# Optimization experiments

Hardware: AMD Instinct MI355X
Metric: run time of the kernel (lower is better)

Reference implementation:

```python
import jax, jax.numpy as jnp
import numpy as np

B, T, D = 2, 2048, 1024
H, DH = 16, 64  # heads, head_dim; inner_dim = H*DH = D
EPS = 1e-6


def _rmsnorm(x, g):
    # torch.nn.RMSNorm over last dim with affine weight g
    return x * jax.lax.rsqrt(jnp.mean(x * x, axis=-1, keepdims=True) + EPS) * g


def _interleaved_rope(x, cos, sin):
    # x: [B, T, D]; pairs (x0, x1) rotated: rot = [-x1, x0, -x3, x2, ...]
    b, t, d = x.shape
    x2 = x.reshape(b, t, d // 2, 2)
    rot = jnp.stack([-x2[..., 1], x2[..., 0]], axis=-1).reshape(b, t, d)
    return x * cos + rot * sin


def setup_inputs() -> dict:
    key = jax.random.key(0)
    ks = jax.random.split(key, 8)
    hidden_states = jax.random.normal(ks[0], (B, T, D), dtype=jnp.float32)
    cos = jax.random.uniform(ks[1], (1, T, D), dtype=jnp.float32)
    sin = jax.random.uniform(ks[2], (1, T, D), dtype=jnp.float32)
    s = 0.02  # init scale for weights
    wq = jax.random.normal(ks[3], (D, D), dtype=jnp.float32) * s
    wk = jax.random.normal(ks[4], (D, D), dtype=jnp.float32) * s
    wv = jax.random.normal(ks[5], (D, D), dtype=jnp.float32) * s
    wo = jax.random.normal(ks[6], (D, D), dtype=jnp.float32) * s
    bq = jnp.zeros((D,), jnp.float32)
    bk = jnp.zeros((D,), jnp.float32)
    bv = jnp.zeros((D,), jnp.float32)
    bo = jnp.zeros((D,), jnp.float32)
    gq = jnp.ones((D,), jnp.float32)
    gk = jnp.ones((D,), jnp.float32)
    return {
        'hidden_states': hidden_states, 'cos': cos, 'sin': sin,
        'wq': wq, 'bq': bq, 'wk': wk, 'bk': bk, 'wv': wv, 'bv': bv,
        'gq': gq, 'gk': gk, 'wo': wo, 'bo': bo,
    }


def reference(hidden_states, cos, sin, wq, bq, wk, bk, wv, bv, gq, gk, wo, bo):
    # QKV projections (weights stored as [in, out]) + RMSNorm(q,k) + RoPE
    q = _interleaved_rope(_rmsnorm(hidden_states @ wq + bq, gq), cos, sin)
    k = _interleaved_rope(_rmsnorm(hidden_states @ wk + bk, gk), cos, sin)
    v = hidden_states @ wv + bv

    # split heads: [B, T, D] -> [B, H, T, DH]
    def split(x):
        return x.reshape(B, T, H, DH).transpose(0, 2, 1, 3)
    q, k, v = split(q), split(k), split(v)

    scale = 1.0 / jnp.sqrt(jnp.float32(DH))
    scores = jnp.einsum('bhqd,bhkd->bhqk', q, k) * scale
    attn = jax.nn.softmax(scores, axis=-1)
    out = jnp.einsum('bhqk,bhkd->bhqd', attn, v)

    # merge heads + output projection
    out = out.transpose(0, 2, 1, 3).reshape(B, T, D)
    return out @ wo + bo
```

## Files before the change

### kernel.cpp

```cpp
#include <hip/hip_runtime.h>

typedef _Float16 f16;
typedef _Float16 f16x8 __attribute__((ext_vector_type(8)));
typedef _Float16 f16x4 __attribute__((ext_vector_type(4)));
typedef _Float16 f16x2 __attribute__((ext_vector_type(2)));
typedef float f32x4 __attribute__((ext_vector_type(4)));

#define MFMA(a, b, c) __builtin_amdgcn_mfma_f32_16x16x32_f16(a, b, c, 0, 0, 0)
#define PKRTZ(a, b) __builtin_bit_cast(f16x2, __builtin_amdgcn_cvt_pkrtz(a, b))

__device__ __forceinline__ void gload16(const void* g, void* l) {
  __builtin_amdgcn_global_load_lds((const __attribute__((address_space(1))) char*)g,
                                   (__attribute__((address_space(3))) char*)l, 16, 0, 0);
}


__global__ __launch_bounds__(256) void k_cvt_hidden(const float* __restrict__ x, f16* __restrict__ y) {
  int i = blockIdx.x * 256 + threadIdx.x;
  float4 v = ((const float4*)x)[i];
  f16x4 h; h[0] = (f16)v.x; h[1] = (f16)v.y; h[2] = (f16)v.z; h[3] = (f16)v.w;
  ((f16x4*)y)[i] = h;
}

__global__ __launch_bounds__(256) void k_cvt_w(const float* __restrict__ w0, const float* __restrict__ w1,
                                               const float* __restrict__ w2, const float* __restrict__ w3,
                                               f16* __restrict__ wt) {
  int z = blockIdx.z;
  const float* w = z == 0 ? w0 : z == 1 ? w1 : z == 2 ? w2 : w3;
  f16* dst = wt + (size_t)z * 1024 * 1024;
  __shared__ float tile[64][65];
  int t = threadIdx.x;
  int k0 = blockIdx.x * 64, n0 = blockIdx.y * 64;
  int cr = t >> 4, cc = (t & 15) * 4;
#pragma unroll
  for (int p = 0; p < 4; p++) {
    int r = cr + p * 16;
    float4 v = *(const float4*)&w[(size_t)(k0 + r) * 1024 + n0 + cc];
    tile[r][cc + 0] = v.x; tile[r][cc + 1] = v.y; tile[r][cc + 2] = v.z; tile[r][cc + 3] = v.w;
  }
  __syncthreads();
#pragma unroll
  for (int p = 0; p < 4; p++) {
    int nn = cr + p * 16;
    f16x4 h;
    h[0] = (f16)tile[cc + 0][nn]; h[1] = (f16)tile[cc + 1][nn];
    h[2] = (f16)tile[cc + 2][nn]; h[3] = (f16)tile[cc + 3][nn];
    *(f16x4*)&dst[(size_t)(n0 + nn) * 1024 + k0 + cc] = h;
  }
}

template <bool OUTF32>
__device__ __forceinline__ void gemm_core(const f16* __restrict__ A, const f16* __restrict__ Wrows,
                                          const float* __restrict__ bias, int m0,
                                          f16* __restrict__ oh, float* __restrict__ of) {
  __shared__ f16 Al[2][128 * 64];
  __shared__ f16 Bl[2][128 * 64];
  const int t = threadIdx.x;
  const int lane = t & 63, wid = t >> 6;
  const int lr = lane & 15, lg = lane >> 4;
  const int wm = wid >> 1, wn = wid & 1;
  const int lrow = lane >> 3;
  const int cb = (((lane & 7) ^ lrow) << 4);

  f32x4 acc[4][4] = {};

  auto stage = [&](int k0, int bs) {
#pragma unroll
    for (int it = 0; it < 4; it++) {
      int rbase = it * 32 + wid * 8;
      int row = rbase + lrow;
      gload16((const char*)&A[(size_t)(m0 + row) * 1024 + k0] + cb, (char*)&Al[bs][0] + rbase * 128);
      gload16((const char*)&Wrows[(size_t)row * 1024 + k0] + cb, (char*)&Bl[bs][0] + rbase * 128);
    }
  };

  stage(0, 0);
  __syncthreads();
  int cur = 0;
  for (int k0 = 0; k0 < 1024; k0 += 64) {
    if (k0 + 64 < 1024) stage(k0 + 64, cur ^ 1);
    f16x8 af[2][4], bf[2][4];
#pragma unroll
    for (int x = 0; x < 4; x++) {
      int ra = wm * 64 + x * 16 + lr;
      int rb = wn * 64 + x * 16 + lr;
#pragma unroll
      for (int kh = 0; kh < 2; kh++) {
        int ca = (kh * 64 + lg * 16) ^ ((lr & 7) << 4);
        af[kh][x] = *(const f16x8*)((char*)&Al[cur][0] + ra * 128 + ca);
        bf[kh][x] = *(const f16x8*)((char*)&Bl[cur][0] + rb * 128 + ca);
      }
    }
    __builtin_amdgcn_s_setprio(1);
#pragma unroll
    for (int kh = 0; kh < 2; kh++)
#pragma unroll
      for (int mt = 0; mt < 4; mt++)
#pragma unroll
        for (int nt = 0; nt < 4; nt++)
          acc[mt][nt] = MFMA(af[kh][mt], bf[kh][nt], acc[mt][nt]);
    __builtin_amdgcn_s_setprio(0);
    __syncthreads();
    cur ^= 1;
  }
#pragma unroll
  for (int mt = 0; mt < 4; mt++) {
#pragma unroll
    for (int nt = 0; nt < 4; nt++) {
      int col = wn * 64 + nt * 16 + lr;
      float bcol = bias[col];
#pragma unroll
      for (int e = 0; e < 4; e++) {
        int row = m0 + wm * 64 + mt * 16 + lg * 4 + e;
        float val = acc[mt][nt][e] + bcol;
        if (OUTF32) of[(size_t)row * 1024 + col] = val;
        else        oh[(size_t)row * 1024 + col] = (f16)val;
      }
    }
  }
}

__global__ __launch_bounds__(256, 2) void k_gemm_qkv(const f16* __restrict__ A, const f16* __restrict__ wt,
                                                     const float* __restrict__ bq, const float* __restrict__ bk,
                                                     const float* __restrict__ bv,
                                                     f16* __restrict__ q, f16* __restrict__ k, f16* __restrict__ v) {
  int n0 = blockIdx.y * 128;
  int zsel = n0 >> 10, cbs = n0 & 1023;
  const float* bias = (zsel == 0 ? bq : zsel == 1 ? bk : bv) + cbs;
  f16* dst = (zsel == 0 ? q : zsel == 1 ? k : v) + cbs;
  gemm_core<false>(A, wt + (size_t)n0 * 1024, bias, blockIdx.x * 128, dst, nullptr);
}

__global__ __launch_bounds__(256, 2) void k_gemm_o(const f16* __restrict__ A, const f16* __restrict__ wt3,
                                                   const float* __restrict__ bo, float* __restrict__ out) {
  int n0 = blockIdx.y * 128;
  gemm_core<true>(A, wt3 + (size_t)n0 * 1024, bo + n0, blockIdx.x * 128, nullptr, out + n0);
}

__global__ __launch_bounds__(256) void k_normrope(f16* __restrict__ qh, f16* __restrict__ kh,
                                                  const float* __restrict__ gq, const float* __restrict__ gk,
                                                  const float* __restrict__ cs, const float* __restrict__ sn) {
  int row = blockIdx.x, which = blockIdx.y;
  f16* buf = which ? kh : qh;
  const float* g = which ? gk : gq;
  int t = threadIdx.x, c4 = t * 4;
  f16x4 xv = *(const f16x4*)&buf[(size_t)row * 1024 + c4];
  float x0 = xv[0], x1 = xv[1], x2 = xv[2], x3 = xv[3];
  float ss = x0 * x0 + x1 * x1 + x2 * x2 + x3 * x3;
#pragma unroll
  for (int off = 1; off < 64; off <<= 1) ss += __shfl_xor(ss, off);
  __shared__ float red[4];
  if ((t & 63) == 0) red[t >> 6] = ss;
  __syncthreads();
  float inv = rsqrtf((red[0] + red[1] + red[2] + red[3]) * (1.0f / 1024.0f) + 1e-6f);
  int tt = row & 2047;
  float4 cv = *(const float4*)&cs[(size_t)tt * 1024 + c4];
  float4 sv = *(const float4*)&sn[(size_t)tt * 1024 + c4];
  float4 gv = *(const float4*)&g[c4];
  float y0 = x0 * inv * gv.x, y1 = x1 * inv * gv.y, y2 = x2 * inv * gv.z, y3 = x3 * inv * gv.w;
  f16x4 ov;
  ov[0] = (f16)(y0 * cv.x - y1 * sv.x);
  ov[1] = (f16)(y1 * cv.y + y0 * sv.y);
  ov[2] = (f16)(y2 * cv.z - y3 * sv.z);
  ov[3] = (f16)(y3 * cv.w + y2 * sv.w);
  *(f16x4*)&buf[(size_t)row * 1024 + c4] = ov;
}

__global__ __launch_bounds__(256) void k_vtrans(const f16* __restrict__ vh, f16* __restrict__ vt) {
  __shared__ f16 tile[64][65];
  int t = threadIdx.x;
  int t0 = blockIdx.x * 64;
  int bh = blockIdx.y;
  int b = bh >> 4, h = bh & 15;
  int rr = t >> 3, c8 = (t & 7) * 8;
#pragma unroll
  for (int p = 0; p < 2; p++) {
    int r = p * 32 + rr;
    f16x8 v = *(const f16x8*)&vh[(size_t)(b * 2048 + t0 + r) * 1024 + h * 64 + c8];
#pragma unroll
    for (int j = 0; j < 8; j++) tile[r][c8 + j] = v[j];
  }
  __syncthreads();
#pragma unroll
  for (int p = 0; p < 2; p++) {
    int dh = p * 32 + rr;
    f16x8 o;
#pragma unroll
    for (int j = 0; j < 8; j++) o[j] = tile[c8 + j][dh];
    *(f16x8*)&vt[((size_t)bh * 64 + dh) * 2048 + t0 + c8] = o;
  }
}

#define ASWZ(row) ((((row) & 3) | (((row) & 8) >> 1)) << 4)

__global__ __launch_bounds__(256, 2) void k_attn(const f16* __restrict__ qh, const f16* __restrict__ kh,
                                                 const f16* __restrict__ vt, f16* __restrict__ ao) {
  __shared__ f16 Kl[2][64 * 64];
  __shared__ f16 Vl[2][64 * 64];
  const int t = threadIdx.x;
  const int lane = t & 63, wid = t >> 6;
  const int lr = lane & 15, lg = lane >> 4;
  const int lgb = lg << 4;
  const int raw = blockIdx.x;
  const int mybh = ((raw & 7) << 2) | ((raw >> 3) & 3);
  const int myq = raw >> 5;
  const int b = mybh >> 4, h = mybh & 15;
  const int q0 = myq * 128 + wid * 32;
  const f16* Qb = qh + ((size_t)(b * 2048 + q0)) * 1024 + h * 64;
  f16x8 qf[2][2];
#pragma unroll
  for (int g = 0; g < 2; g++) {
    qf[g][0] = *(const f16x8*)&Qb[(size_t)(g * 16 + lr) * 1024 + lg * 8];
    qf[g][1] = *(const f16x8*)&Qb[(size_t)(g * 16 + lr) * 1024 + 32 + lg * 8];
  }
  const f16* Kg = kh + ((size_t)b * 2048) * 1024 + h * 64;
  const f16* Vg = vt + ((size_t)mybh) * 64 * 2048;
  const int lrow = lane >> 3;
  const int sg = (lane & 7) << 4;
  const float sc = 0.125f * 1.44269504088896340736f;
  float m[2] = {-1e30f, -1e30f};
  f32x4 acc[2][4] = {};
  f32x4 accl[2] = {};
  const f16 ov1 = (lr == 0) ? (f16)1.0f : (f16)0.0f;
  const f16x8 onesf = {ov1, ov1, ov1, ov1, ov1, ov1, ov1, ov1};

  auto stage = [&](int kvo, int bs) {
#pragma unroll
    for (int i = 0; i < 2; i++) {
      int rbase = (i * 4 + wid) * 8;
      int row = rbase + lrow;
      int cswz = sg ^ ASWZ(row);
      gload16((const char*)(Kg + (size_t)(kvo + row) * 1024) + cswz, (char*)&Kl[bs][0] + rbase * 128);
      gload16((const char*)(Vg + (size_t)row * 2048 + kvo) + cswz, (char*)&Vl[bs][0] + rbase * 128);
    }
  };

  stage(0, 0);
  __syncthreads();
  int cur = 0;

  for (int kv0 = 0; kv0 < 2048; kv0 += 64) {
    if (kv0 + 64 < 2048) stage(kv0 + 64, cur ^ 1);
    const char* Kb = (const char*)&Kl[cur][0];
    const char* Vb = (const char*)&Vl[cur][0];

    f32x4 s[2][4];
    __builtin_amdgcn_s_setprio(1);
#pragma unroll
    for (int ks = 0; ks < 4; ks++) {
      int key = ((lr >> 2) << 3) + (lr & 3) + ((ks & 1) << 2) + ((ks >> 1) << 5);
      int sw = ASWZ(key);
      f16x8 kf0 = *(const f16x8*)(Kb + key * 128 + (lgb ^ sw));
      f16x8 kf1 = *(const f16x8*)(Kb + key * 128 + ((64 + lgb) ^ sw));
#pragma unroll
      for (int g = 0; g < 2; g++) {
        f32x4 z = {};
        z = MFMA(kf0, qf[g][0], z);
        z = MFMA(kf1, qf[g][1], z);
        s[g][ks] = z;
      }
    }
    __builtin_amdgcn_s_setprio(0);

    union U { f16x8 v; f16x2 h[4]; } u[2][2];
#pragma unroll
    for (int g = 0; g < 2; g++) {
      float smax = fmaxf(fmaxf(s[g][0][0], s[g][0][1]), s[g][0][2]);
      smax = fmaxf(fmaxf(smax, s[g][0][3]), s[g][1][0]);
      smax = fmaxf(fmaxf(smax, s[g][1][1]), s[g][1][2]);
      smax = fmaxf(fmaxf(smax, s[g][1][3]), s[g][2][0]);
      smax = fmaxf(fmaxf(smax, s[g][2][1]), s[g][2][2]);
      smax = fmaxf(fmaxf(smax, s[g][2][3]), s[g][3][0]);
      smax = fmaxf(fmaxf(smax, s[g][3][1]), s[g][3][2]);
      smax = fmaxf(smax, s[g][3][3]);
      smax = fmaxf(smax, __shfl_xor(smax, 16));
      smax = fmaxf(smax, __shfl_xor(smax, 32));
      float smc = smax * sc;

      if (!__all(smc - m[g] <= 8.f)) {
        float mn = fmaxf(m[g], smc);
        float al = exp2f(m[g] - mn);
        m[g] = mn;
        float alq[4];
#pragma unroll
        for (int e = 0; e < 4; e++) alq[e] = __shfl(al, lg * 4 + e);
#pragma unroll
        for (int ds = 0; ds < 4; ds++)
#pragma unroll
          for (int e = 0; e < 4; e++) acc[g][ds][e] *= alq[e];
#pragma unroll
        for (int e = 0; e < 4; e++) accl[g][e] *= alq[e];
      }

#pragma unroll
      for (int ks = 0; ks < 4; ks++) {
        float p0 = exp2f(fmaf(s[g][ks][0], sc, -m[g]));
        float p1 = exp2f(fmaf(s[g][ks][1], sc, -m[g]));
        float p2 = exp2f(fmaf(s[g][ks][2], sc, -m[g]));
        float p3 = exp2f(fmaf(s[g][ks][3], sc, -m[g]));
        u[g][ks >> 1].h[(ks & 1) * 2 + 0] = PKRTZ(p0, p1);
        u[g][ks >> 1].h[(ks & 1) * 2 + 1] = PKRTZ(p2, p3);
      }
    }

    __builtin_amdgcn_s_setprio(1);
#pragma unroll
    for (int ds = 0; ds < 4; ds++) {
      int vrow = ds * 16 + lr;
      int sw = ASWZ(vrow);
      f16x8 vf0 = *(const f16x8*)(Vb + vrow * 128 + (lgb ^ sw));
      f16x8 vf1 = *(const f16x8*)(Vb + vrow * 128 + ((64 + lgb) ^ sw));
#pragma unroll
      for (int g = 0; g < 2; g++) {
        acc[g][ds] = MFMA(u[g][0].v, vf0, acc[g][ds]);
        acc[g][ds] = MFMA(u[g][1].v, vf1, acc[g][ds]);
      }
    }
#pragma unroll
    for (int g = 0; g < 2; g++) {
      accl[g] = MFMA(u[g][0].v, onesf, accl[g]);
      accl[g] = MFMA(u[g][1].v, onesf, accl[g]);
    }
    __builtin_amdgcn_s_setprio(0);

    __syncthreads();
    cur ^= 1;
  }

#pragma unroll
  for (int g = 0; g < 2; g++) {
#pragma unroll
    for (int e = 0; e < 4; e++) {
      float lf = 1.f / __shfl(accl[g][e], lg << 4);
      size_t row = (size_t)(b * 2048 + q0 + g * 16 + lg * 4 + e);
#pragma unroll
      for (int ds = 0; ds < 4; ds++)
        ao[row * 1024 + h * 64 + ds * 16 + lr] = (f16)(acc[g][ds][e] * lf);
    }
  }
}

extern "C" void kernel_launch(void* const* d_in, const int* in_sizes, int n_in,
                              void* d_out, int out_size, void* d_ws, size_t ws_size,
                              hipStream_t stream) {
  const float* hid  = (const float*)d_in[0];
  const float* cosb = (const float*)d_in[1];
  const float* sinb = (const float*)d_in[2];
  const float* wq = (const float*)d_in[3];
  const float* bq = (const float*)d_in[4];
  const float* wk = (const float*)d_in[5];
  const float* bk = (const float*)d_in[6];
  const float* wv = (const float*)d_in[7];
  const float* bv = (const float*)d_in[8];
  const float* gq = (const float*)d_in[9];
  const float* gk = (const float*)d_in[10];
  const float* wo = (const float*)d_in[11];
  const float* bo = (const float*)d_in[12];
  float* out = (float*)d_out;

  char* ws = (char*)d_ws;
  f16* aH  = (f16*)(ws);
  f16* wt  = (f16*)(ws + ((size_t)8 << 20));
  f16* qh  = (f16*)(ws + ((size_t)16 << 20));
  f16* khb = (f16*)(ws + ((size_t)24 << 20));
  f16* vhb = (f16*)(ws + ((size_t)32 << 20));
  f16* vtb = (f16*)(ws + ((size_t)40 << 20));
  f16* ao  = (f16*)(ws + ((size_t)48 << 20));

  k_cvt_hidden<<<dim3(4096), dim3(256), 0, stream>>>(hid, aH);
  k_cvt_w<<<dim3(16, 16, 4), dim3(256), 0, stream>>>(wq, wk, wv, wo, wt);
  k_gemm_qkv<<<dim3(32, 24), dim3(256), 0, stream>>>(aH, wt, bq, bk, bv, qh, khb, vhb);
  k_normrope<<<dim3(4096, 2), dim3(256), 0, stream>>>(qh, khb, gq, gk, cosb, sinb);
  k_vtrans<<<dim3(32, 32), dim3(256), 0, stream>>>(vhb, vtb);
  k_attn<<<dim3(512), dim3(256), 0, stream>>>(qh, khb, vtb, ao);
  k_gemm_o<<<dim3(32, 8), dim3(256), 0, stream>>>(ao, wt + (size_t)3 * 1024 * 1024, bo, out);
}
```

Measured before the change: 143.2 us.

## Split attention KV range in two halves and merge partials with log-sum-exp

The attention kernel now splits each query tile's key/value range into two halves handled by separate blocks, doubling the grid from 512 to 1024 blocks and raising the occupancy hint to 4 blocks per SM. Each half writes a normalized partial output plus its running max and row sum, and a new merge kernel combines the two halves with log-sum-exp weights. The aim is to fill more of the GPU's compute units during attention. The cost is an extra kernel launch, extra global traffic for the partial outputs (stored in reused workspace buffers), and possible register spilling under the tighter launch bounds.

Measured after the change: 145.1 us. No clear change (+1.3%).

```diff
diff --git a/kernel.cpp b/kernel.cpp
--- a/kernel.cpp
+++ b/kernel.cpp
@@ -193,8 +193,10 @@
 
 #define ASWZ(row) ((((row) & 3) | (((row) & 8) >> 1)) << 4)
 
-__global__ __launch_bounds__(256, 2) void k_attn(const f16* __restrict__ qh, const f16* __restrict__ kh,
-                                                 const f16* __restrict__ vt, f16* __restrict__ ao) {
+__global__ __launch_bounds__(256, 4) void k_attn(const f16* __restrict__ qh, const f16* __restrict__ kh,
+                                                 const f16* __restrict__ vt,
+                                                 f16* __restrict__ op0, f16* __restrict__ op1,
+                                                 float* __restrict__ ml) {
   __shared__ f16 Kl[2][64 * 64];
   __shared__ f16 Vl[2][64 * 64];
   const int t = threadIdx.x;
@@ -203,9 +205,12 @@
   const int lgb = lg << 4;
   const int raw = blockIdx.x;
   const int mybh = ((raw & 7) << 2) | ((raw >> 3) & 3);
-  const int myq = raw >> 5;
+  const int half = (raw >> 5) & 1;
+  const int myq = raw >> 6;
   const int b = mybh >> 4, h = mybh & 15;
   const int q0 = myq * 128 + wid * 32;
+  const int kvbase = half << 10;
+  f16* __restrict__ op = half ? op1 : op0;
   const f16* Qb = qh + ((size_t)(b * 2048 + q0)) * 1024 + h * 64;
   f16x8 qf[2][2];
 #pragma unroll
@@ -235,12 +240,13 @@
     }
   };
 
-  stage(0, 0);
+  stage(kvbase, 0);
   __syncthreads();
   int cur = 0;
 
-  for (int kv0 = 0; kv0 < 2048; kv0 += 64) {
-    if (kv0 + 64 < 2048) stage(kv0 + 64, cur ^ 1);
+  for (int c = 0; c < 16; c++) {
+    int kv0 = kvbase + c * 64;
+    if (c + 1 < 16) stage(kv0 + 64, cur ^ 1);
     const char* Kb = (const char*)&Kl[cur][0];
     const char* Vb = (const char*)&Vl[cur][0];
 
@@ -329,15 +335,43 @@
 
 #pragma unroll
   for (int g = 0; g < 2; g++) {
+    int qglob = mybh * 2048 + q0 + g * 16;
+    if (lg == 0)
+      ml[(size_t)((half << 16) + qglob + lr) * 2 + 0] = m[g];
+    if (lr == 0) {
+#pragma unroll
+      for (int e = 0; e < 4; e++)
+        ml[(size_t)((half << 16) + qglob + lg * 4 + e) * 2 + 1] = accl[g][e];
+    }
 #pragma unroll
     for (int e = 0; e < 4; e++) {
       float lf = 1.f / __shfl(accl[g][e], lg << 4);
       size_t row = (size_t)(b * 2048 + q0 + g * 16 + lg * 4 + e);
 #pragma unroll
       for (int ds = 0; ds < 4; ds++)
-        ao[row * 1024 + h * 64 + ds * 16 + lr] = (f16)(acc[g][ds][e] * lf);
-    }
-  }
+        op[row * 1024 + h * 64 + ds * 16 + lr] = (f16)(acc[g][ds][e] * lf);
+    }
+  }
+}
+
+__global__ __launch_bounds__(256) void k_merge(const f16* __restrict__ op0, const f16* __restrict__ op1,
+                                               const float* __restrict__ ml, f16* __restrict__ ao) {
+  int i = blockIdx.x * 256 + threadIdx.x;
+  int qid = i >> 3, seg = i & 7;
+  float m0 = ml[(size_t)qid * 2], l0 = ml[(size_t)qid * 2 + 1];
+  float m1 = ml[(size_t)(65536 + qid) * 2], l1 = ml[(size_t)(65536 + qid) * 2 + 1];
+  float mm = fmaxf(m0, m1);
+  float w0 = l0 * exp2f(m0 - mm), w1 = l1 * exp2f(m1 - mm);
+  float inv = 1.f / (w0 + w1);
+  w0 *= inv; w1 *= inv;
+  int bh = qid >> 11, tt = qid & 2047;
+  size_t addr = (((size_t)(bh >> 4) * 2048 + tt) * 1024 + (bh & 15) * 64 + seg * 8) / 8;
+  f16x8 a = ((const f16x8*)op0)[addr];
+  f16x8 bb = ((const f16x8*)op1)[addr];
+  f16x8 o;
+#pragma unroll
+  for (int j = 0; j < 8; j++) o[j] = (f16)(w0 * (float)a[j] + w1 * (float)bb[j]);
+  ((f16x8*)ao)[addr] = o;
 }
 
 extern "C" void kernel_launch(void* const* d_in, const int* in_sizes, int n_in,
@@ -366,12 +400,14 @@
   f16* vhb = (f16*)(ws + ((size_t)32 << 20));
   f16* vtb = (f16*)(ws + ((size_t)40 << 20));
   f16* ao  = (f16*)(ws + ((size_t)48 << 20));
+  float* ml = (float*)(ws + ((size_t)56 << 20));
 
   k_cvt_hidden<<<dim3(4096), dim3(256), 0, stream>>>(hid, aH);
   k_cvt_w<<<dim3(16, 16, 4), dim3(256), 0, stream>>>(wq, wk, wv, wo, wt);
   k_gemm_qkv<<<dim3(32, 24), dim3(256), 0, stream>>>(aH, wt, bq, bk, bv, qh, khb, vhb);
   k_normrope<<<dim3(4096, 2), dim3(256), 0, stream>>>(qh, khb, gq, gk, cosb, sinb);
   k_vtrans<<<dim3(32, 32), dim3(256), 0, stream>>>(vhb, vtb);
-  k_attn<<<dim3(512), dim3(256), 0, stream>>>(qh, khb, vtb, ao);
+  k_attn<<<dim3(1024), dim3(256), 0, stream>>>(qh, khb, vtb, vhb, aH, ml);
+  k_merge<<<dim3(2048), dim3(256), 0, stream>>>(vhb, aH, ml, ao);
   k_gemm_o<<<dim3(32, 8), dim3(256), 0, stream>>>(ao, wt + (size_t)3 * 1024 * 1024, bo, out);
 }
```

## Rewrite QKV GEMM as 256x256 tile with 8-wave ping-pong LDS pipeline

Applied to the files above, without the earlier changes.

The QKV projection GEMM moves from 128x128 tiles with 4 waves and double buffering to 256x256 tiles with 8 waves. Each tile is split into four 128-row half-tiles per K step, and global-to-LDS loads are interleaved with MFMA quadrants under explicit barriers and waitcnts. A block-index swizzle groups neighbouring tiles for L2 reuse. The aim is to raise data reuse per LDS byte and hide load latency. The costs are a grid of only 192 blocks on 256 CUs (under one wave of work) and a fragile hand-written synchronisation schedule.

Result: no change. 142.8 us (-0.3%).

```diff
diff --git a/kernel.cpp b/kernel.cpp
--- a/kernel.cpp
+++ b/kernel.cpp
@@ -8,6 +8,8 @@
 
 #define MFMA(a, b, c) __builtin_amdgcn_mfma_f32_16x16x32_f16(a, b, c, 0, 0, 0)
 #define PKRTZ(a, b) __builtin_bit_cast(f16x2, __builtin_amdgcn_cvt_pkrtz(a, b))
+#define BARRAW() do { asm volatile("" ::: "memory"); __builtin_amdgcn_s_barrier(); asm volatile("" ::: "memory"); } while (0)
+#define WAITLGKM0() do { asm volatile("s_waitcnt lgkmcnt(0)" ::: "memory"); __builtin_amdgcn_sched_barrier(0); } while (0)
 
 __device__ __forceinline__ void gload16(const void* g, void* l) {
   __builtin_amdgcn_global_load_lds((const __attribute__((address_space(1))) char*)g,
@@ -49,10 +51,144 @@
   }
 }
 
-template <bool OUTF32>
-__device__ __forceinline__ void gemm_core(const f16* __restrict__ A, const f16* __restrict__ Wrows,
-                                          const float* __restrict__ bias, int m0,
-                                          f16* __restrict__ oh, float* __restrict__ of) {
+__global__ __launch_bounds__(512, 1) void k_gemm_qkv(const f16* __restrict__ A, const f16* __restrict__ wt,
+                                                     const float* __restrict__ bq, const float* __restrict__ bk,
+                                                     const float* __restrict__ bv,
+                                                     f16* __restrict__ q, f16* __restrict__ k, f16* __restrict__ v) {
+  __shared__ f16 L[8][128 * 64];
+  const int t = threadIdx.x;
+  const int lane = t & 63, wid = t >> 6;
+  const int lr = lane & 15, lg = lane >> 4;
+  const int wm = wid >> 2, wn = wid & 3;
+  const int lrow = lane >> 3;
+  const int cb = (((lane & 7) ^ lrow) << 4);
+  const int bid = blockIdx.x;
+  const int x = bid & 7, loc = bid >> 3;
+  const int bx = (x & 3) * 4 + (loc & 3);
+  const int by = (x >> 2) * 6 + (loc >> 2);
+  const int m0 = bx * 256, n0 = by * 256;
+  const f16* Ag = A + (size_t)m0 * 1024;
+  const f16* Wr = wt + (size_t)n0 * 1024;
+  const int zsel = by >> 2, cbs = (by & 3) * 256;
+  const float* bias = (zsel == 0 ? bq : zsel == 1 ? bk : bv) + cbs;
+  f16* dst = (zsel == 0 ? q : zsel == 1 ? k : v) + cbs;
+
+  f32x4 acc[8][4] = {};
+
+  auto stageH = [&](int par, int mat, int h, int tk) {
+    const f16* base = (mat ? Wr : Ag) + (size_t)(h * 128) * 1024 + (tk << 6);
+    char* slot = (char*)&L[par * 4 + mat * 2 + h][0];
+#pragma unroll
+    for (int j = 0; j < 2; j++) {
+      int rbase = j * 64 + wid * 8;
+      gload16((const char*)&base[(size_t)(rbase + lrow) * 1024] + cb, slot + rbase * 128);
+    }
+  };
+  auto loadA = [&](int par, int h, f16x8 (&af)[8]) {
+    const char* S = (const char*)&L[par * 4 + h][0];
+#pragma unroll
+    for (int mt = 0; mt < 4; mt++) {
+      int ra = wm * 64 + mt * 16 + lr;
+#pragma unroll
+      for (int kh = 0; kh < 2; kh++)
+        af[mt * 2 + kh] = *(const f16x8*)(S + ra * 128 + ((kh * 64 + lg * 16) ^ ((lr & 7) << 4)));
+    }
+  };
+  auto loadB = [&](int par, int h, f16x8 (&bf)[4]) {
+    const char* S = (const char*)&L[par * 4 + 2 + h][0];
+#pragma unroll
+    for (int nt = 0; nt < 2; nt++) {
+      int rb = wn * 32 + nt * 16 + lr;
+#pragma unroll
+      for (int kh = 0; kh < 2; kh++)
+        bf[nt * 2 + kh] = *(const f16x8*)(S + rb * 128 + ((kh * 64 + lg * 16) ^ ((lr & 7) << 4)));
+    }
+  };
+  auto mfma16 = [&](int mh, int nh, f16x8 (&af)[8], f16x8 (&bf)[4]) {
+    __builtin_amdgcn_s_setprio(1);
+#pragma unroll
+    for (int kh = 0; kh < 2; kh++)
+#pragma unroll
+      for (int mt = 0; mt < 4; mt++)
+#pragma unroll
+        for (int nt = 0; nt < 2; nt++)
+          acc[mh * 4 + mt][nh * 2 + nt] = MFMA(af[mt * 2 + kh], bf[nt * 2 + kh], acc[mh * 4 + mt][nh * 2 + nt]);
+    __builtin_amdgcn_s_setprio(0);
+  };
+
+  stageH(0, 0, 0, 0); stageH(0, 1, 0, 0); stageH(0, 1, 1, 0); stageH(0, 0, 1, 0);
+  stageH(1, 0, 0, 1); stageH(1, 1, 1, 1); stageH(1, 0, 1, 1);
+  asm volatile("s_waitcnt vmcnt(6)" ::: "memory");
+  BARRAW();
+
+  f16x8 afA[8], afB[8], bfA[4], bfB[4];
+  for (int i = 0; i < 8; i++) {
+    const int t2 = 2 * i + 2, t3 = 2 * i + 3;
+    const bool pre = (i < 7);
+    loadA(0, 0, afA); loadB(0, 0, bfA);
+    stageH(1, 1, 0, 2 * i + 1);
+    BARRAW(); WAITLGKM0();
+    mfma16(0, 0, afA, bfA);
+    BARRAW();
+    loadB(0, 1, bfB);
+    if (pre) stageH(0, 0, 0, t2);
+    BARRAW(); WAITLGKM0();
+    mfma16(0, 1, afA, bfB);
+    BARRAW();
+    loadA(0, 1, afB);
+    if (pre) stageH(0, 1, 1, t2);
+    BARRAW(); WAITLGKM0();
+    mfma16(1, 1, afB, bfB);
+    BARRAW();
+    loadB(0, 0, bfA);
+    if (pre) stageH(0, 0, 1, t2);
+    asm volatile("s_waitcnt vmcnt(4)" ::: "memory");
+    BARRAW(); WAITLGKM0();
+    mfma16(1, 0, afB, bfA);
+    BARRAW();
+    loadA(1, 0, afA); loadB(1, 0, bfA);
+    if (pre) stageH(0, 1, 0, t2);
+    BARRAW(); WAITLGKM0();
+    mfma16(0, 0, afA, bfA);
+    BARRAW();
+    loadB(1, 1, bfB);
+    if (pre) stageH(1, 0, 0, t3);
+    BARRAW(); WAITLGKM0();
+    mfma16(0, 1, afA, bfB);
+    BARRAW();
+    loadA(1, 1, afB);
+    if (pre) stageH(1, 1, 1, t3);
+    BARRAW(); WAITLGKM0();
+    mfma16(1, 1, afB, bfB);
+    BARRAW();
+    loadB(1, 0, bfA);
+    if (pre) stageH(1, 0, 1, t3);
+    asm volatile("s_waitcnt vmcnt(4)" ::: "memory");
+    BARRAW(); WAITLGKM0();
+    mfma16(1, 0, afB, bfA);
+    BARRAW();
+  }
+
+#pragma unroll
+  for (int mh = 0; mh < 2; mh++)
+#pragma unroll
+    for (int mt = 0; mt < 4; mt++)
+#pragma unroll
+      for (int nh = 0; nh < 2; nh++)
+#pragma unroll
+        for (int nt = 0; nt < 2; nt++) {
+          int col = nh * 128 + wn * 32 + nt * 16 + lr;
+          float bcol = bias[col];
+#pragma unroll
+          for (int e = 0; e < 4; e++) {
+            int row = m0 + mh * 128 + wm * 64 + mt * 16 + lg * 4 + e;
+            dst[(size_t)row * 1024 + col] = (f16)(acc[mh * 4 + mt][nh * 2 + nt][e] + bcol);
+          }
+        }
+}
+
+__global__ __launch_bounds__(256, 2) void k_gemm_o(const f16* __restrict__ A, const f16* __restrict__ Wrows3,
+                                                   const float* __restrict__ bo, float* __restrict__ out) {
   __shared__ f16 Al[2][128 * 64];
   __shared__ f16 Bl[2][128 * 64];
   const int t = threadIdx.x;
@@ -61,6 +197,10 @@
   const int wm = wid >> 1, wn = wid & 1;
   const int lrow = lane >> 3;
   const int cb = (((lane & 7) ^ lrow) << 4);
+  const int m0 = blockIdx.x * 128, n0 = blockIdx.y * 128;
+  const f16* Wrows = Wrows3 + (size_t)n0 * 1024;
+  const float* bias = bo + n0;
+  float* of = out + n0;
 
   f32x4 acc[4][4] = {};
 
@@ -81,14 +221,14 @@
     if (k0 + 64 < 1024) stage(k0 + 64, cur ^ 1);
     f16x8 af[2][4], bf[2][4];
 #pragma unroll
-    for (int x = 0; x < 4; x++) {
-      int ra = wm * 64 + x * 16 + lr;
-      int rb = wn * 64 + x * 16 + lr;
+    for (int xx = 0; xx < 4; xx++) {
+      int ra = wm * 64 + xx * 16 + lr;
+      int rb = wn * 64 + xx * 16 + lr;
 #pragma unroll
       for (int kh = 0; kh < 2; kh++) {
         int ca = (kh * 64 + lg * 16) ^ ((lr & 7) << 4);
-        af[kh][x] = *(const f16x8*)((char*)&Al[cur][0] + ra * 128 + ca);
-        bf[kh][x] = *(const f16x8*)((char*)&Bl[cur][0] + rb * 128 + ca);
+        af[kh][xx] = *(const f16x8*)((char*)&Al[cur][0] + ra * 128 + ca);
+        bf[kh][xx] = *(const f16x8*)((char*)&Bl[cur][0] + rb * 128 + ca);
       }
     }
     __builtin_amdgcn_s_setprio(1);
@@ -112,29 +252,10 @@
 #pragma unroll
       for (int e = 0; e < 4; e++) {
         int row = m0 + wm * 64 + mt * 16 + lg * 4 + e;
-        float val = acc[mt][nt][e] + bcol;
-        if (OUTF32) of[(size_t)row * 1024 + col] = val;
-        else        oh[(size_t)row * 1024 + col] = (f16)val;
-      }
-    }
-  }
-}
-
-__global__ __launch_bounds__(256, 2) void k_gemm_qkv(const f16* __restrict__ A, const f16* __restrict__ wt,
-                                                     const float* __restrict__ bq, const float* __restrict__ bk,
-                                                     const float* __restrict__ bv,
-                                                     f16* __restrict__ q, f16* __restrict__ k, f16* __restrict__ v) {
-  int n0 = blockIdx.y * 128;
-  int zsel = n0 >> 10, cbs = n0 & 1023;
-  const float* bias = (zsel == 0 ? bq : zsel == 1 ? bk : bv) + cbs;
-  f16* dst = (zsel == 0 ? q : zsel == 1 ? k : v) + cbs;
-  gemm_core<false>(A, wt + (size_t)n0 * 1024, bias, blockIdx.x * 128, dst, nullptr);
-}
-
-__global__ __launch_bounds__(256, 2) void k_gemm_o(const f16* __restrict__ A, const f16* __restrict__ wt3,
-                                                   const float* __restrict__ bo, float* __restrict__ out) {
-  int n0 = blockIdx.y * 128;
-  gemm_core<true>(A, wt3 + (size_t)n0 * 1024, bo + n0, blockIdx.x * 128, nullptr, out + n0);
+        of[(size_t)row * 1024 + col] = acc[mt][nt][e] + bcol;
+      }
+    }
+  }
 }
 
 __global__ __launch_bounds__(256) void k_normrope(f16* __restrict__ qh, f16* __restrict__ kh,
@@ -369,7 +490,7 @@
 
   k_cvt_hidden<<<dim3(4096), dim3(256), 0, stream>>>(hid, aH);
   k_cvt_w<<<dim3(16, 16, 4), dim3(256), 0, stream>>>(wq, wk, wv, wo, wt);
-  k_gemm_qkv<<<dim3(32, 24), dim3(256), 0, stream>>>(aH, wt, bq, bk, bv, qh, khb, vhb);
+  k_gemm_qkv<<<dim3(192), dim3(512), 0, stream>>>(aH, wt, bq, bk, bv, qh, khb, vhb);
   k_normrope<<<dim3(4096, 2), dim3(256), 0, stream>>>(qh, khb, gq, gk, cosb, sinb);
   k_vtrans<<<dim3(32, 32), dim3(256), 0, stream>>>(vhb, vtb);
   k_attn<<<dim3(512), dim3(256), 0, stream>>>(qh, khb, vtb, ao);
```

## Fuse hidden-state conversion and V transpose into QKV GEMM, merge q/k normrope

Applied to the files above, without the earlier changes.

The QKV GEMM now reads fp32 hidden states directly, converting them to fp16 in registers while staging into LDS. The separate conversion kernel goes away, and the A-tile load now goes through registers instead of the direct global-to-LDS path. The V block of the GEMM writes its output already transposed into the per-head layout attention expects, which removes the separate transpose kernel. The norm+RoPE kernel now handles q and k for a row in one block, sharing the cos/sin loads. The costs are fp32 A reads every tile, extra register pressure, and scattered 8-byte transposed stores for V.

After: 153.5 us. 7.2% more time.

```diff
diff --git a/kernel.cpp b/kernel.cpp
--- a/kernel.cpp
+++ b/kernel.cpp
@@ -14,13 +14,6 @@
                                    (__attribute__((address_space(3))) char*)l, 16, 0, 0);
 }
 
-
-__global__ __launch_bounds__(256) void k_cvt_hidden(const float* __restrict__ x, f16* __restrict__ y) {
-  int i = blockIdx.x * 256 + threadIdx.x;
-  float4 v = ((const float4*)x)[i];
-  f16x4 h; h[0] = (f16)v.x; h[1] = (f16)v.y; h[2] = (f16)v.z; h[3] = (f16)v.w;
-  ((f16x4*)y)[i] = h;
-}
 
 __global__ __launch_bounds__(256) void k_cvt_w(const float* __restrict__ w0, const float* __restrict__ w1,
                                                const float* __restrict__ w2, const float* __restrict__ w3,
@@ -49,10 +42,124 @@
   }
 }
 
-template <bool OUTF32>
-__device__ __forceinline__ void gemm_core(const f16* __restrict__ A, const f16* __restrict__ Wrows,
-                                          const float* __restrict__ bias, int m0,
-                                          f16* __restrict__ oh, float* __restrict__ of) {
+__global__ __launch_bounds__(256, 2) void k_gemm_qkv(const float* __restrict__ A, const f16* __restrict__ wt,
+                                                     const float* __restrict__ bq, const float* __restrict__ bk,
+                                                     const float* __restrict__ bv,
+                                                     f16* __restrict__ q, f16* __restrict__ k, f16* __restrict__ vt) {
+  __shared__ f16 Al[2][128 * 64];
+  __shared__ f16 Bl[2][128 * 64];
+  const int t = threadIdx.x;
+  const int lane = t & 63, wid = t >> 6;
+  const int lr = lane & 15, lg = lane >> 4;
+  const int wm = wid >> 1, wn = wid & 1;
+  const int lrow = lane >> 3;
+  const int scol8 = (lane & 7) ^ lrow;
+  const int m0 = blockIdx.x * 128;
+  const int n0 = blockIdx.y * 128;
+  const int zsel = n0 >> 10, cbs = n0 & 1023;
+  const f16* Wrows = wt + (size_t)n0 * 1024;
+  const float* bias = (zsel == 0 ? bq : zsel == 1 ? bk : bv) + cbs;
+
+  f32x4 acc[4][4] = {};
+  float4 ar[4][2];
+
+  auto loadA = [&](int k0) {
+#pragma unroll
+    for (int it = 0; it < 4; it++) {
+      int row = it * 32 + wid * 8 + lrow;
+      const float* ap = &A[(size_t)(m0 + row) * 1024 + k0 + scol8 * 8];
+      ar[it][0] = *(const float4*)ap;
+      ar[it][1] = *(const float4*)(ap + 4);
+    }
+  };
+  auto writeA = [&](int bs) {
+#pragma unroll
+    for (int it = 0; it < 4; it++) {
+      f16x8 h;
+#pragma unroll
+      for (int j = 0; j < 4; j++) {
+        h[j]     = (f16)(&ar[it][0].x)[j];
+        h[4 + j] = (f16)(&ar[it][1].x)[j];
+      }
+      int row = it * 32 + wid * 8 + lrow;
+      *(f16x8*)((char*)&Al[bs][0] + row * 128 + ((lane & 7) << 4)) = h;
+    }
+  };
+  auto stageB = [&](int k0, int bs) {
+#pragma unroll
+    for (int it = 0; it < 4; it++) {
+      int rbase = it * 32 + wid * 8;
+      gload16((const char*)&Wrows[(size_t)(rbase + lrow) * 1024 + k0] + (scol8 << 4),
+              (char*)&Bl[bs][0] + rbase * 128);
+    }
+  };
+
+  loadA(0); stageB(0, 0); writeA(0);
+  __syncthreads();
+  int cur = 0;
+  for (int k0 = 0; k0 < 1024; k0 += 64) {
+    bool pre = (k0 + 64 < 1024);
+    if (pre) { loadA(k0 + 64); stageB(k0 + 64, cur ^ 1); }
+    f16x8 af[2][4], bf[2][4];
+#pragma unroll
+    for (int x = 0; x < 4; x++) {
+      int ra = wm * 64 + x * 16 + lr;
+      int rb = wn * 64 + x * 16 + lr;
+#pragma unroll
+      for (int kh = 0; kh < 2; kh++) {
+        int ca = (kh * 64 + lg * 16) ^ ((lr & 7) << 4);
+        af[kh][x] = *(const f16x8*)((char*)&Al[cur][0] + ra * 128 + ca);
+        bf[kh][x] = *(const f16x8*)((char*)&Bl[cur][0] + rb * 128 + ca);
+      }
+    }
+    __builtin_amdgcn_s_setprio(1);
+#pragma unroll
+    for (int kh = 0; kh < 2; kh++)
+#pragma unroll
+      for (int mt = 0; mt < 4; mt++)
+#pragma unroll
+        for (int nt = 0; nt < 4; nt++)
+          acc[mt][nt] = MFMA(af[kh][mt], bf[kh][nt], acc[mt][nt]);
+    __builtin_amdgcn_s_setprio(0);
+    if (pre) writeA(cur ^ 1);
+    __syncthreads();
+    cur ^= 1;
+  }
+
+  if (zsel < 2) {
+    f16* oh = (zsel == 0 ? q : k) + cbs;
+#pragma unroll
+    for (int mt = 0; mt < 4; mt++)
+#pragma unroll
+      for (int nt = 0; nt < 4; nt++) {
+        int col = wn * 64 + nt * 16 + lr;
+        float bcol = bias[col];
+#pragma unroll
+        for (int e = 0; e < 4; e++) {
+          int row = m0 + wm * 64 + mt * 16 + lg * 4 + e;
+          oh[(size_t)row * 1024 + col] = (f16)(acc[mt][nt][e] + bcol);
+        }
+      }
+  } else {
+#pragma unroll
+    for (int mt = 0; mt < 4; mt++)
+#pragma unroll
+      for (int nt = 0; nt < 4; nt++) {
+        int col = cbs + wn * 64 + nt * 16 + lr;
+        float bcol = bias[wn * 64 + nt * 16 + lr];
+        int h = col >> 6, dh = col & 63;
+        int row = m0 + wm * 64 + mt * 16 + lg * 4;
+        int b = row >> 11, tt = row & 2047;
+        f16x4 o;
+#pragma unroll
+        for (int e = 0; e < 4; e++) o[e] = (f16)(acc[mt][nt][e] + bcol);
+        *(f16x4*)&vt[((size_t)(b * 16 + h) * 64 + dh) * 2048 + tt] = o;
+      }
+  }
+}
+
+__global__ __launch_bounds__(256, 2) void k_gemm_o(const f16* __restrict__ A, const f16* __restrict__ Wrows3,
+                                                   const float* __restrict__ bo, float* __restrict__ out) {
   __shared__ f16 Al[2][128 * 64];
   __shared__ f16 Bl[2][128 * 64];
   const int t = threadIdx.x;
@@ -61,6 +168,10 @@
   const int wm = wid >> 1, wn = wid & 1;
   const int lrow = lane >> 3;
   const int cb = (((lane & 7) ^ lrow) << 4);
+  const int m0 = blockIdx.x * 128, n0 = blockIdx.y * 128;
+  const f16* Wrows = Wrows3 + (size_t)n0 * 1024;
+  const float* bias = bo + n0;
+  float* of = out + n0;
 
   f32x4 acc[4][4] = {};
 
@@ -81,14 +192,14 @@
     if (k0 + 64 < 1024) stage(k0 + 64, cur ^ 1);
     f16x8 af[2][4], bf[2][4];
 #pragma unroll
-    for (int x = 0; x < 4; x++) {
-      int ra = wm * 64 + x * 16 + lr;
-      int rb = wn * 64 + x * 16 + lr;
+    for (int xx = 0; xx < 4; xx++) {
+      int ra = wm * 64 + xx * 16 + lr;
+      int rb = wn * 64 + xx * 16 + lr;
 #pragma unroll
       for (int kh = 0; kh < 2; kh++) {
         int ca = (kh * 64 + lg * 16) ^ ((lr & 7) << 4);
-        af[kh][x] = *(const f16x8*)((char*)&Al[cur][0] + ra * 128 + ca);
-        bf[kh][x] = *(const f16x8*)((char*)&Bl[cur][0] + rb * 128 + ca);
+        af[kh][xx] = *(const f16x8*)((char*)&Al[cur][0] + ra * 128 + ca);
+        bf[kh][xx] = *(const f16x8*)((char*)&Bl[cur][0] + rb * 128 + ca);
       }
     }
     __builtin_amdgcn_s_setprio(1);
@@ -112,83 +223,48 @@
 #pragma unroll
       for (int e = 0; e < 4; e++) {
         int row = m0 + wm * 64 + mt * 16 + lg * 4 + e;
-        float val = acc[mt][nt][e] + bcol;
-        if (OUTF32) of[(size_t)row * 1024 + col] = val;
-        else        oh[(size_t)row * 1024 + col] = (f16)val;
-      }
-    }
-  }
-}
-
-__global__ __launch_bounds__(256, 2) void k_gemm_qkv(const f16* __restrict__ A, const f16* __restrict__ wt,
-                                                     const float* __restrict__ bq, const float* __restrict__ bk,
-                                                     const float* __restrict__ bv,
-                                                     f16* __restrict__ q, f16* __restrict__ k, f16* __restrict__ v) {
-  int n0 = blockIdx.y * 128;
-  int zsel = n0 >> 10, cbs = n0 & 1023;
-  const float* bias = (zsel == 0 ? bq : zsel == 1 ? bk : bv) + cbs;
-  f16* dst = (zsel == 0 ? q : zsel == 1 ? k : v) + cbs;
-  gemm_core<false>(A, wt + (size_t)n0 * 1024, bias, blockIdx.x * 128, dst, nullptr);
-}
-
-__global__ __launch_bounds__(256, 2) void k_gemm_o(const f16* __restrict__ A, const f16* __restrict__ wt3,
-                                                   const float* __restrict__ bo, float* __restrict__ out) {
-  int n0 = blockIdx.y * 128;
-  gemm_core<true>(A, wt3 + (size_t)n0 * 1024, bo + n0, blockIdx.x * 128, nullptr, out + n0);
+        of[(size_t)row * 1024 + col] = acc[mt][nt][e] + bcol;
+      }
+    }
+  }
 }
 
 __global__ __launch_bounds__(256) void k_normrope(f16* __restrict__ qh, f16* __restrict__ kh,
                                                   const float* __restrict__ gq, const float* __restrict__ gk,
                                                   const float* __restrict__ cs, const float* __restrict__ sn) {
-  int row = blockIdx.x, which = blockIdx.y;
-  f16* buf = which ? kh : qh;
-  const float* g = which ? gk : gq;
+  int row = blockIdx.x;
   int t = threadIdx.x, c4 = t * 4;
-  f16x4 xv = *(const f16x4*)&buf[(size_t)row * 1024 + c4];
-  float x0 = xv[0], x1 = xv[1], x2 = xv[2], x3 = xv[3];
-  float ss = x0 * x0 + x1 * x1 + x2 * x2 + x3 * x3;
-#pragma unroll
-  for (int off = 1; off < 64; off <<= 1) ss += __shfl_xor(ss, off);
-  __shared__ float red[4];
-  if ((t & 63) == 0) red[t >> 6] = ss;
+  f16x4 xq = *(const f16x4*)&qh[(size_t)row * 1024 + c4];
+  f16x4 xk = *(const f16x4*)&kh[(size_t)row * 1024 + c4];
+  float q0 = xq[0], q1 = xq[1], q2 = xq[2], q3 = xq[3];
+  float k0 = xk[0], k1 = xk[1], k2 = xk[2], k3 = xk[3];
+  float sq = q0 * q0 + q1 * q1 + q2 * q2 + q3 * q3;
+  float sk = k0 * k0 + k1 * k1 + k2 * k2 + k3 * k3;
+#pragma unroll
+  for (int off = 1; off < 64; off <<= 1) { sq += __shfl_xor(sq, off); sk += __shfl_xor(sk, off); }
+  __shared__ float redq[4], redk[4];
+  if ((t & 63) == 0) { redq[t >> 6] = sq; redk[t >> 6] = sk; }
   __syncthreads();
-  float inv = rsqrtf((red[0] + red[1] + red[2] + red[3]) * (1.0f / 1024.0f) + 1e-6f);
+  float invq = rsqrtf((redq[0] + redq[1] + redq[2] + redq[3]) * (1.0f / 1024.0f) + 1e-6f);
+  float invk = rsqrtf((redk[0] + redk[1] + redk[2] + redk[3]) * (1.0f / 1024.0f) + 1e-6f);
   int tt = row & 2047;
   float4 cv = *(const float4*)&cs[(size_t)tt * 1024 + c4];
   float4 sv = *(const float4*)&sn[(size_t)tt * 1024 + c4];
-  float4 gv = *(const float4*)&g[c4];
-  float y0 = x0 * inv * gv.x, y1 = x1 * inv * gv.y, y2 = x2 * inv * gv.z, y3 = x3 * inv * gv.w;
-  f16x4 ov;
-  ov[0] = (f16)(y0 * cv.x - y1 * sv.x);
-  ov[1] = (f16)(y1 * cv.y + y0 * sv.y);
-  ov[2] = (f16)(y2 * cv.z - y3 * sv.z);
-  ov[3] = (f16)(y3 * cv.w + y2 * sv.w);
-  *(f16x4*)&buf[(size_t)row * 1024 + c4] = ov;
-}
-
-__global__ __launch_bounds__(256) void k_vtrans(const f16* __restrict__ vh, f16* __restrict__ vt) {
-  __shared__ f16 tile[64][65];
-  int t = threadIdx.x;
-  int t0 = blockIdx.x * 64;
-  int bh = blockIdx.y;
-  int b = bh >> 4, h = bh & 15;
-  int rr = t >> 3, c8 = (t & 7) * 8;
-#pragma unroll
-  for (int p = 0; p < 2; p++) {
-    int r = p * 32 + rr;
-    f16x8 v = *(const f16x8*)&vh[(size_t)(b * 2048 + t0 + r) * 1024 + h * 64 + c8];
-#pragma unroll
-    for (int j = 0; j < 8; j++) tile[r][c8 + j] = v[j];
-  }
-  __syncthreads();
-#pragma unroll
-  for (int p = 0; p < 2; p++) {
-    int dh = p * 32 + rr;
-    f16x8 o;
-#pragma unroll
-    for (int j = 0; j < 8; j++) o[j] = tile[c8 + j][dh];
-    *(f16x8*)&vt[((size_t)bh * 64 + dh) * 2048 + t0 + c8] = o;
-  }
+  float4 gqv = *(const float4*)&gq[c4];
+  float4 gkv = *(const float4*)&gk[c4];
+  float a0 = q0 * invq * gqv.x, a1 = q1 * invq * gqv.y, a2 = q2 * invq * gqv.z, a3 = q3 * invq * gqv.w;
+  float b0 = k0 * invk * gkv.x, b1 = k1 * invk * gkv.y, b2 = k2 * invk * gkv.z, b3 = k3 * invk * gkv.w;
+  f16x4 oq, ok;
+  oq[0] = (f16)(a0 * cv.x - a1 * sv.x);
+  oq[1] = (f16)(a1 * cv.y + a0 * sv.y);
+  oq[2] = (f16)(a2 * cv.z - a3 * sv.z);
+  oq[3] = (f16)(a3 * cv.w + a2 * sv.w);
+  ok[0] = (f16)(b0 * cv.x - b1 * sv.x);
+  ok[1] = (f16)(b1 * cv.y + b0 * sv.y);
+  ok[2] = (f16)(b2 * cv.z - b3 * sv.z);
+  ok[3] = (f16)(b3 * cv.w + b2 * sv.w);
+  *(f16x4*)&qh[(size_t)row * 1024 + c4] = oq;
+  *(f16x4*)&kh[(size_t)row * 1024 + c4] = ok;
 }
 
 #define ASWZ(row) ((((row) & 3) | (((row) & 8) >> 1)) << 4)
@@ -359,19 +435,15 @@
   float* out = (float*)d_out;
 
   char* ws = (char*)d_ws;
-  f16* aH  = (f16*)(ws);
-  f16* wt  = (f16*)(ws + ((size_t)8 << 20));
-  f16* qh  = (f16*)(ws + ((size_t)16 << 20));
-  f16* khb = (f16*)(ws + ((size_t)24 << 20));
-  f16* vhb = (f16*)(ws + ((size_t)32 << 20));
-  f16* vtb = (f16*)(ws + ((size_t)40 << 20));
-  f16* ao  = (f16*)(ws + ((size_t)48 << 20));
-
-  k_cvt_hidden<<<dim3(4096), dim3(256), 0, stream>>>(hid, aH);
+  f16* wt  = (f16*)(ws);
+  f16* qh  = (f16*)(ws + ((size_t)8 << 20));
+  f16* khb = (f16*)(ws + ((size_t)16 << 20));
+  f16* vtb = (f16*)(ws + ((size_t)24 << 20));
+  f16* ao  = (f16*)(ws + ((size_t)32 << 20));
+
   k_cvt_w<<<dim3(16, 16, 4), dim3(256), 0, stream>>>(wq, wk, wv, wo, wt);
-  k_gemm_qkv<<<dim3(32, 24), dim3(256), 0, stream>>>(aH, wt, bq, bk, bv, qh, khb, vhb);
-  k_normrope<<<dim3(4096, 2), dim3(256), 0, stream>>>(qh, khb, gq, gk, cosb, sinb);
-  k_vtrans<<<dim3(32, 32), dim3(256), 0, stream>>>(vhb, vtb);
+  k_gemm_qkv<<<dim3(32, 24), dim3(256), 0, stream>>>(hid, wt, bq, bk, bv, qh, khb, vtb);
+  k_normrope<<<dim3(4096), dim3(256), 0, stream>>>(qh, khb, gq, gk, cosb, sinb);
   k_attn<<<dim3(512), dim3(256), 0, stream>>>(qh, khb, vtb, ao);
   k_gemm_o<<<dim3(32, 8), dim3(256), 0, stream>>>(ao, wt + (size_t)3 * 1024 * 1024, bo, out);
 }
```
